# Kernel optimization log

Measured on AMD Instinct MI355X. Metric: run time of the kernel, lower is better.

## Reference

```python
import jax, jax.numpy as jnp
import numpy as np

LN_EPS = 1e-5


def _layernorm(x, g, b):
    m = x.mean(-1, keepdims=True)
    v = ((x - m) ** 2).mean(-1, keepdims=True)
    return (x - m) * jax.lax.rsqrt(v + LN_EPS) * g + b


def setup_inputs() -> dict:
    key = jax.random.key(0)
    ks = jax.random.split(key, 8)
    bs, dsc, qlen, dm, nh, dc, dff = 16, 8, 512, 256, 16, 128, 1024
    dk = dm // nh  # 16
    s = 0.02
    return {
        "src": jax.random.normal(ks[0], (bs, dsc, qlen, dm), jnp.float32),
        "router": jax.random.normal(ks[1], (1, nh, dc, dk), jnp.float32) * 0.1,
        "Wk_w": jax.random.normal(ks[2], (nh * dk, dm), jnp.float32) * s,
        "Wk_b": jnp.zeros((nh * dk,), jnp.float32),
        "out_w": jax.random.normal(ks[3], (dm, nh * dk), jnp.float32) * s,
        "out_b": jnp.zeros((dm,), jnp.float32),
        "m_expand": jax.random.normal(ks[4], (1, qlen, dc), jnp.float32) * 0.1,
        "pos_embd": jax.random.normal(ks[5], (1, 1, dc, dm), jnp.float32) * 0.02,
        "scale_tf": jnp.ones((1, dsc, 1, 1), jnp.float32),
        "ln1_g": jnp.ones((dm,), jnp.float32),
        "ln1_b": jnp.zeros((dm,), jnp.float32),
        "ff1_w": jax.random.normal(ks[6], (dff, dm), jnp.float32) * s,
        "ff1_b": jnp.zeros((dff,), jnp.float32),
        "ff2_w": jax.random.normal(ks[7], (dm, dff), jnp.float32) * s,
        "ff2_b": jnp.zeros((dm,), jnp.float32),
        "ln2_g": jnp.ones((dm,), jnp.float32),
        "ln2_b": jnp.zeros((dm,), jnp.float32),
    }


def reference(src, router, Wk_w, Wk_b, out_w, out_b, m_expand, pos_embd,
              scale_tf, ln1_g, ln1_b, ff1_w, ff1_b, ff2_w, ff2_b, ln2_g, ln2_b):
    bs, dsc, qlen, dm = src.shape
    _, nh, dc, dk = router.shape
    scale = jnp.asarray(dk, src.dtype) ** -0.5

    # flatten (d_share_corr, q_len) into attended sequence S = dsc*qlen
    x = src.reshape(bs, dsc * qlen, dm)
    k = (x @ Wk_w.T + Wk_b).reshape(bs, dsc * qlen, nh, dk)  # [b,S,h,dk]

    # learned-router compressed attention: Q = router (shared across batch), V = K (b_share_kv)
    scores = jnp.einsum('hcd,bshd->bhcs', router[0], k) * scale  # [b,h,dc,S]
    attn = jax.nn.softmax(scores, axis=-1)
    ctx = jnp.einsum('bhcs,bshd->bchd', attn, k).reshape(bs, dc, nh * dk)

    ar = (ctx @ out_w.T + out_b)[:, None] + pos_embd  # [b,1,dc,dm]

    # expand compressed tokens back to q_len, scale per transform
    src2 = jnp.einsum('qc,bxcd->bxqd', m_expand[0], ar) * scale_tf  # [b,dsc,q,dm]
    y = _layernorm(src + src2, ln1_g, ln1_b)

    # FFN (exact gelu, as torch default)
    h = jax.nn.gelu(y @ ff1_w.T + ff1_b, approximate=False)
    y = _layernorm(y + (h @ ff2_w.T + ff2_b), ln2_g, ln2_b)
    return y
```

## Files before the change

kernel.cpp:

```cpp
#include <hip/hip_runtime.h>
#include <math.h>

typedef unsigned short u16;
typedef unsigned int u32;
typedef __bf16 b16x8 __attribute__((ext_vector_type(8)));
typedef float f32x4 __attribute__((ext_vector_type(4)));

#define BS 16
#define DSC 8
#define QL 512
#define DM 256
#define NH 16
#define DKH 16
#define DC 128
#define DFF 1024
#define S_TOT 4096
#define R_TOT 65536
#define ATT_SCALE 0.36067376022224085f

static __device__ __forceinline__ u16 f2bf(float f) {
  u32 u = __float_as_uint(f);
  u += 0x7fffu + ((u >> 16) & 1u);
  return (u16)(u >> 16);
}

static __device__ __forceinline__ uint4 pack8(float4 a, float4 b) {
  uint4 o;
  o.x = (u32)f2bf(a.x) | ((u32)f2bf(a.y) << 16);
  o.y = (u32)f2bf(a.z) | ((u32)f2bf(a.w) << 16);
  o.z = (u32)f2bf(b.x) | ((u32)f2bf(b.y) << 16);
  o.w = (u32)f2bf(b.z) | ((u32)f2bf(b.w) << 16);
  return o;
}

__global__ void cvt_kernel(const float* __restrict__ in, u16* __restrict__ outp, int n4) {
  for (int i = blockIdx.x * blockDim.x + threadIdx.x; i < n4; i += gridDim.x * blockDim.x) {
    float4 v = *(const float4*)(in + (size_t)i * 4);
    uint2 o;
    o.x = (u32)f2bf(v.x) | ((u32)f2bf(v.y) << 16);
    o.y = (u32)f2bf(v.z) | ((u32)f2bf(v.w) << 16);
    *(uint2*)(outp + (size_t)i * 4) = o;
  }
}

__global__ void transp_kernel(const float* __restrict__ w, float* __restrict__ wt) {
  int i = blockIdx.x * 256 + threadIdx.x;
  int k = i >> 8, n = i & 255;
  wt[i] = w[n * 256 + k];
}

template <int EPI, int AF32, int NTY>
__global__ __launch_bounds__(256) void gemm_bf16(
    const void* __restrict__ Av, const u16* __restrict__ B,
    const float* __restrict__ bias, const float* __restrict__ resid,
    void* __restrict__ out, int K, int ldo) {
  __shared__ __align__(16) u16 As[128 * 40];
  __shared__ __align__(16) u16 Bs[128 * 40];
  const int g = blockIdx.x;
  const int xcd = g & 7, tt = g >> 3;
  const int m0 = (xcd * 64 + tt / NTY) * 128;
  const int n0 = (tt % NTY) * 128;
  const int tid = threadIdx.x;
  const int w = tid >> 6, lane = tid & 63;
  const int wm = (w >> 1) * 64, wn = (w & 1) * 64;
  const int fr = lane & 15, fq = lane >> 4;

  f32x4 acc[4][4];
#pragma unroll
  for (int i = 0; i < 4; i++)
#pragma unroll
    for (int j = 0; j < 4; j++) acc[i][j] = (f32x4){0.f, 0.f, 0.f, 0.f};

  const u16* Bg = B + (size_t)n0 * K;
  const int r0 = tid >> 2, o0 = (tid & 3) * 8;
  const int r1 = r0 + 64;

  for (int k0 = 0; k0 < K; k0 += 32) {
    uint4 a0, a1;
    if (AF32) {
      const float* Agf = (const float*)Av + (size_t)m0 * K;
      float4 l0 = *(const float4*)(Agf + (size_t)r0 * K + k0 + o0);
      float4 h0 = *(const float4*)(Agf + (size_t)r0 * K + k0 + o0 + 4);
      float4 l1 = *(const float4*)(Agf + (size_t)r1 * K + k0 + o0);
      float4 h1 = *(const float4*)(Agf + (size_t)r1 * K + k0 + o0 + 4);
      a0 = pack8(l0, h0);
      a1 = pack8(l1, h1);
    } else {
      const u16* Ag = (const u16*)Av + (size_t)m0 * K;
      a0 = *(const uint4*)(Ag + (size_t)r0 * K + k0 + o0);
      a1 = *(const uint4*)(Ag + (size_t)r1 * K + k0 + o0);
    }
    uint4 b0 = *(const uint4*)(Bg + (size_t)r0 * K + k0 + o0);
    uint4 b1 = *(const uint4*)(Bg + (size_t)r1 * K + k0 + o0);
    __syncthreads();
    *(uint4*)&As[r0 * 40 + o0] = a0;
    *(uint4*)&As[r1 * 40 + o0] = a1;
    *(uint4*)&Bs[r0 * 40 + o0] = b0;
    *(uint4*)&Bs[r1 * 40 + o0] = b1;
    __syncthreads();

    uint4 af[4], bf[4];
#pragma unroll
    for (int i = 0; i < 4; i++) {
      af[i] = *(const uint4*)&As[(wm + i * 16 + fr) * 40 + fq * 8];
      bf[i] = *(const uint4*)&Bs[(wn + i * 16 + fr) * 40 + fq * 8];
    }
#pragma unroll
    for (int mi = 0; mi < 4; mi++)
#pragma unroll
      for (int ni = 0; ni < 4; ni++)
        acc[mi][ni] = __builtin_amdgcn_mfma_f32_16x16x32_bf16(
            __builtin_bit_cast(b16x8, af[mi]), __builtin_bit_cast(b16x8, bf[ni]),
            acc[mi][ni], 0, 0, 0);
  }

#pragma unroll
  for (int ni = 0; ni < 4; ni++) {
    const int gc = n0 + wn + ni * 16 + fr;
    const float bv = bias[gc];
#pragma unroll
    for (int mi = 0; mi < 4; mi++) {
#pragma unroll
      for (int r = 0; r < 4; r++) {
        const int gr = m0 + wm + mi * 16 + fq * 4 + r;
        float v = acc[mi][ni][r] + bv;
        if (EPI == 1) v = 0.5f * v * (1.f + erff(v * 0.70710678118f));
        if (EPI == 2) {
          v += resid[(size_t)gr * ldo + gc];
          ((float*)out)[(size_t)gr * ldo + gc] = v;
        } else {
          ((u16*)out)[(size_t)gr * ldo + gc] = f2bf(v);
        }
      }
    }
  }
}

__global__ __launch_bounds__(256) void attn_mfma(const u16* __restrict__ kbf,
                                                 const float* __restrict__ router,
                                                 float* __restrict__ ctxb) {
  const int blk = blockIdx.x;
  const int bh = blk >> 1, chalf = blk & 1;
  const int b = bh >> 4, h = bh & 15;
  const int tid = threadIdx.x, w = tid >> 6, lane = tid & 63;
  const int l15 = lane & 15, lg = lane >> 4;

  __shared__ __align__(16) u16 Pl[4][64 * 40];
  __shared__ __align__(16) u16 kTl[4][16 * 40];
  __shared__ float ctxp[4][64][16];
  __shared__ float lp[4][64];

  uint4 rB[4];
  {
    const float* rb = router + ((size_t)h * DC + chalf * 64) * 16;
#pragma unroll
    for (int nf = 0; nf < 4; nf++) {
      if (lg < 2) {
        const float* p = rb + (nf * 16 + l15) * 16 + lg * 8;
        float4 lo = *(const float4*)p;
        float4 hi = *(const float4*)(p + 4);
        lo.x *= ATT_SCALE; lo.y *= ATT_SCALE; lo.z *= ATT_SCALE; lo.w *= ATT_SCALE;
        hi.x *= ATT_SCALE; hi.y *= ATT_SCALE; hi.z *= ATT_SCALE; hi.w *= ATT_SCALE;
        rB[nf] = pack8(lo, hi);
      } else {
        rB[nf] = make_uint4(0, 0, 0, 0);
      }
    }
  }

  const u16* kg = kbf + (size_t)b * S_TOT * (NH * DKH) + h * 16;

  f32x4 ctx[4];
#pragma unroll
  for (int i = 0; i < 4; i++) ctx[i] = (f32x4){0.f, 0.f, 0.f, 0.f};
  float ladd[4] = {0.f, 0.f, 0.f, 0.f};

  for (int tt = w; tt < 128; tt += 4) {
    const int s0 = tt * 32;
    uint4 kA[2];
#pragma unroll
    for (int mf = 0; mf < 2; mf++)
      kA[mf] = (lg < 2)
                   ? *(const uint4*)(kg + (size_t)(s0 + mf * 16 + l15) * 256 + lg * 8)
                   : make_uint4(0, 0, 0, 0);
    {
      const int sl = lane & 31, dh = lane >> 5;
      uint4 kv = *(const uint4*)(kg + (size_t)(s0 + sl) * 256 + dh * 8);
      const u16* pv = (const u16*)&kv;
#pragma unroll
      for (int jj = 0; jj < 8; jj++) kTl[w][(dh * 8 + jj) * 40 + sl] = pv[jj];
    }
    f32x4 sc[2][4];
#pragma unroll
    for (int mf = 0; mf < 2; mf++)
#pragma unroll
      for (int nf = 0; nf < 4; nf++)
        sc[mf][nf] = __builtin_amdgcn_mfma_f32_16x16x32_bf16(
            __builtin_bit_cast(b16x8, kA[mf]), __builtin_bit_cast(b16x8, rB[nf]),
            (f32x4){0.f, 0.f, 0.f, 0.f}, 0, 0, 0);
#pragma unroll
    for (int mf = 0; mf < 2; mf++)
#pragma unroll
      for (int nf = 0; nf < 4; nf++) {
        float p0 = exp2f(sc[mf][nf][0]);
        float p1 = exp2f(sc[mf][nf][1]);
        float p2 = exp2f(sc[mf][nf][2]);
        float p3 = exp2f(sc[mf][nf][3]);
        ladd[nf] += (p0 + p1) + (p2 + p3);
        uint2 pk;
        pk.x = (__float_as_uint(p0) >> 16) | (__float_as_uint(p1) & 0xffff0000u);
        pk.y = (__float_as_uint(p2) >> 16) | (__float_as_uint(p3) & 0xffff0000u);
        *(uint2*)&Pl[w][(nf * 16 + l15) * 40 + mf * 16 + lg * 4] = pk;
      }
    uint4 kB = *(const uint4*)&kTl[w][l15 * 40 + lg * 8];
#pragma unroll
    for (int mfc = 0; mfc < 4; mfc++) {
      uint4 pA = *(const uint4*)&Pl[w][(mfc * 16 + l15) * 40 + lg * 8];
      ctx[mfc] = __builtin_amdgcn_mfma_f32_16x16x32_bf16(
          __builtin_bit_cast(b16x8, pA), __builtin_bit_cast(b16x8, kB), ctx[mfc],
          0, 0, 0);
    }
  }

#pragma unroll
  for (int nf = 0; nf < 4; nf++) {
    float v = ladd[nf];
    v += __shfl_xor(v, 16);
    v += __shfl_xor(v, 32);
    ladd[nf] = v;
  }
  if (lane < 16) {
#pragma unroll
    for (int nf = 0; nf < 4; nf++) lp[w][nf * 16 + lane] = ladd[nf];
  }
#pragma unroll
  for (int mfc = 0; mfc < 4; mfc++)
#pragma unroll
    for (int r = 0; r < 4; r++) ctxp[w][mfc * 16 + lg * 4 + r][l15] = ctx[mfc][r];
  __syncthreads();
#pragma unroll
  for (int i = 0; i < 4; i++) {
    const int idx = tid + i * 256;
    const int c = idx >> 4, d = idx & 15;
    const float L = lp[0][c] + lp[1][c] + lp[2][c] + lp[3][c];
    const float V = ctxp[0][c][d] + ctxp[1][c][d] + ctxp[2][c][d] + ctxp[3][c][d];
    ctxb[((size_t)b * DC + chalf * 64 + c) * (NH * DKH) + h * 16 + d] = V / L;
  }
}

__global__ __launch_bounds__(256) void ar_kernel(const float* __restrict__ ctxb,
                                                 const float* __restrict__ owT,
                                                 const float* __restrict__ ob,
                                                 const float* __restrict__ pos,
                                                 float* __restrict__ ar) {
  const int b = blockIdx.x, g = blockIdx.y, n = threadIdx.x;
  __shared__ float cl[8][256];
#pragma unroll
  for (int j = 0; j < 8; j++)
    cl[j][n] = ctxb[((size_t)b * DC + g * 8 + j) * 256 + n];
  __syncthreads();
  float acc[8];
#pragma unroll
  for (int j = 0; j < 8; j++) acc[j] = ob[n] + pos[(size_t)(g * 8 + j) * 256 + n];
  for (int k = 0; k < 256; k++) {
    float wv = owT[(size_t)k * 256 + n];
#pragma unroll
    for (int j = 0; j < 8; j++) acc[j] += cl[j][k] * wv;
  }
#pragma unroll
  for (int j = 0; j < 8; j++) ar[((size_t)b * DC + g * 8 + j) * 256 + n] = acc[j];
}

__global__ __launch_bounds__(256) void texp_kernel(const float* __restrict__ me,
                                                   const float* __restrict__ ar,
                                                   float* __restrict__ tb) {
  const int b = blockIdx.x, qg = blockIdx.y, d = threadIdx.x;
  __shared__ float ml[16][128];
  const int q0 = qg * 16;
  for (int i = threadIdx.x; i < 16 * 128; i += 256) {
    int qq = i >> 7, c = i & 127;
    ml[qq][c] = me[(size_t)(q0 + qq) * 128 + c];
  }
  __syncthreads();
  float acc[16];
#pragma unroll
  for (int qq = 0; qq < 16; qq++) acc[qq] = 0.f;
  for (int c = 0; c < 128; c++) {
    float v = ar[((size_t)b * DC + c) * 256 + d];
#pragma unroll
    for (int qq = 0; qq < 16; qq++) acc[qq] += ml[qq][c] * v;
  }
#pragma unroll
  for (int qq = 0; qq < 16; qq++)
    tb[((size_t)(b * QL + q0 + qq)) * 256 + d] = acc[qq];
}

__global__ __launch_bounds__(256) void ln1_kernel(
    const float* __restrict__ src, const float* __restrict__ tbuf,
    const float* __restrict__ stf, const float* __restrict__ g,
    const float* __restrict__ bb, float* __restrict__ yout) {
  const int w = threadIdx.x >> 6, lane = threadIdx.x & 63;
  const int r = blockIdx.x * 4 + w;
  const int b = r >> 12, x = (r >> 9) & 7, q = r & 511;
  const size_t base = (size_t)r * DM + lane * 4;
  float4 s4 = *(const float4*)(src + base);
  float4 t4 = *(const float4*)(tbuf + ((size_t)(b * QL + q) * DM + lane * 4));
  const float sc = stf[x];
  float v0 = s4.x + sc * t4.x, v1 = s4.y + sc * t4.y;
  float v2 = s4.z + sc * t4.z, v3 = s4.w + sc * t4.w;
  float sum = v0 + v1 + v2 + v3;
  float sq = v0 * v0 + v1 * v1 + v2 * v2 + v3 * v3;
#pragma unroll
  for (int off = 32; off; off >>= 1) {
    sum += __shfl_xor(sum, off);
    sq += __shfl_xor(sq, off);
  }
  const float mean = sum * (1.f / DM);
  const float var = sq * (1.f / DM) - mean * mean;
  const float rs = rsqrtf(var + 1e-5f);
  float4 gv = *(const float4*)(g + lane * 4);
  float4 bv = *(const float4*)(bb + lane * 4);
  float4 o;
  o.x = (v0 - mean) * rs * gv.x + bv.x;
  o.y = (v1 - mean) * rs * gv.y + bv.y;
  o.z = (v2 - mean) * rs * gv.z + bv.z;
  o.w = (v3 - mean) * rs * gv.w + bv.w;
  *(float4*)(yout + base) = o;
}

__global__ __launch_bounds__(256) void ln2_kernel(float* __restrict__ io,
                                                  const float* __restrict__ g,
                                                  const float* __restrict__ bb) {
  const int w = threadIdx.x >> 6, lane = threadIdx.x & 63;
  const int r = blockIdx.x * 4 + w;
  const size_t base = (size_t)r * DM + lane * 4;
  float4 v4 = *(const float4*)(io + base);
  float sum = v4.x + v4.y + v4.z + v4.w;
  float sq = v4.x * v4.x + v4.y * v4.y + v4.z * v4.z + v4.w * v4.w;
#pragma unroll
  for (int off = 32; off; off >>= 1) {
    sum += __shfl_xor(sum, off);
    sq += __shfl_xor(sq, off);
  }
  const float mean = sum * (1.f / DM);
  const float var = sq * (1.f / DM) - mean * mean;
  const float rs = rsqrtf(var + 1e-5f);
  float4 gv = *(const float4*)(g + lane * 4);
  float4 bv = *(const float4*)(bb + lane * 4);
  float4 o;
  o.x = (v4.x - mean) * rs * gv.x + bv.x;
  o.y = (v4.y - mean) * rs * gv.y + bv.y;
  o.z = (v4.z - mean) * rs * gv.z + bv.z;
  o.w = (v4.w - mean) * rs * gv.w + bv.w;
  *(float4*)(io + base) = o;
}

extern "C" void kernel_launch(void* const* d_in, const int* in_sizes, int n_in,
                              void* d_out, int out_size, void* d_ws, size_t ws_size,
                              hipStream_t stream) {
  const float* src = (const float*)d_in[0];
  const float* router = (const float*)d_in[1];
  const float* wk_w = (const float*)d_in[2];
  const float* wk_b = (const float*)d_in[3];
  const float* out_w = (const float*)d_in[4];
  const float* out_b = (const float*)d_in[5];
  const float* m_exp = (const float*)d_in[6];
  const float* pos = (const float*)d_in[7];
  const float* stf = (const float*)d_in[8];
  const float* ln1g = (const float*)d_in[9];
  const float* ln1b = (const float*)d_in[10];
  const float* f1w = (const float*)d_in[11];
  const float* f1b = (const float*)d_in[12];
  const float* f2w = (const float*)d_in[13];
  const float* f2b = (const float*)d_in[14];
  const float* ln2g = (const float*)d_in[15];
  const float* ln2b = (const float*)d_in[16];
  float* out = (float*)d_out;

  unsigned char* ws = (unsigned char*)d_ws;
  u16* k_bf = (u16*)(ws + 0);
  u16* h_bf = (u16*)(ws + 33554432);
  u16* wkw_bf = (u16*)(ws + 167772160);
  u16* f1w_bf = (u16*)(ws + 167903232);
  u16* f2w_bf = (u16*)(ws + 168427520);
  float* owT = (float*)(ws + 168951808);
  float* ctxb = (float*)(ws + 169213952);
  float* arb = (float*)(ws + 171311104);
  float* tb = (float*)(ws + 173408256);

  cvt_kernel<<<64, 256, 0, stream>>>(wk_w, wkw_bf, 256 * 256 / 4);
  cvt_kernel<<<256, 256, 0, stream>>>(f1w, f1w_bf, DFF * DM / 4);
  cvt_kernel<<<256, 256, 0, stream>>>(f2w, f2w_bf, DM * DFF / 4);
  transp_kernel<<<256, 256, 0, stream>>>(out_w, owT);

  gemm_bf16<0, 1, 2><<<1024, 256, 0, stream>>>(src, wkw_bf, wk_b, nullptr,
                                               k_bf, DM, DM);
  attn_mfma<<<512, 256, 0, stream>>>(k_bf, router, ctxb);
  ar_kernel<<<dim3(16, 16), 256, 0, stream>>>(ctxb, owT, out_b, pos, arb);
  texp_kernel<<<dim3(16, 32), 256, 0, stream>>>(m_exp, arb, tb);
  ln1_kernel<<<16384, 256, 0, stream>>>(src, tb, stf, ln1g, ln1b, out);

  gemm_bf16<1, 1, 8><<<4096, 256, 0, stream>>>(out, f1w_bf, f1b, nullptr,
                                               h_bf, DM, DFF);
  gemm_bf16<2, 0, 2><<<1024, 256, 0, stream>>>(h_bf, f2w_bf, f2b, out,
                                               out, DFF, DM);
  ln2_kernel<<<16384, 256, 0, stream>>>(out, ln2g, ln2b);
}
```

Before: 492.3 us.

## Load GEMM tiles via global_load_lds, pre-convert A to bf16, stage output stores

The GEMM now loads A and B tiles straight into LDS with global_load_lds, which drops the register round trip and one barrier per k-step. To make that possible, the fp32 A operands are converted to bf16 up front: src gets a new conversion pass, and ln1 writes a bf16 copy of its output. The bf16 epilogue is staged through LDS so global stores are coalesced 16-byte writes. The cost is an extra full read and write of src, an extra bf16 write in ln1, and an unpadded LDS layout that may cause bank conflicts.

```diff
diff --git a/kernel.cpp b/kernel.cpp
--- a/kernel.cpp
+++ b/kernel.cpp
@@ -33,6 +33,12 @@
   return o;
 }
 
+static __device__ __forceinline__ void gload16(const u16* g, u16* l) {
+  __builtin_amdgcn_global_load_lds(
+      (const __attribute__((address_space(1))) void*)g,
+      (__attribute__((address_space(3))) void*)l, 16, 0, 0);
+}
+
 __global__ void cvt_kernel(const float* __restrict__ in, u16* __restrict__ outp, int n4) {
   for (int i = blockIdx.x * blockDim.x + threadIdx.x; i < n4; i += gridDim.x * blockDim.x) {
     float4 v = *(const float4*)(in + (size_t)i * 4);
@@ -49,13 +55,14 @@
   wt[i] = w[n * 256 + k];
 }
 
-template <int EPI, int AF32, int NTY>
+template <int EPI, int NTY>
 __global__ __launch_bounds__(256) void gemm_bf16(
-    const void* __restrict__ Av, const u16* __restrict__ B,
+    const u16* __restrict__ A, const u16* __restrict__ B,
     const float* __restrict__ bias, const float* __restrict__ resid,
     void* __restrict__ out, int K, int ldo) {
-  __shared__ __align__(16) u16 As[128 * 40];
-  __shared__ __align__(16) u16 Bs[128 * 40];
+  __shared__ __align__(16) u16 smem[8192];
+  u16* As = smem;
+  u16* Bs = smem + 4096;
   const int g = blockIdx.x;
   const int xcd = g & 7, tt = g >> 3;
   const int m0 = (xcd * 64 + tt / NTY) * 128;
@@ -71,39 +78,30 @@
 #pragma unroll
     for (int j = 0; j < 4; j++) acc[i][j] = (f32x4){0.f, 0.f, 0.f, 0.f};
 
+  const int jr = lane >> 2, jc = (lane & 3) * 8;
+  const u16* Ag = A + (size_t)m0 * K;
   const u16* Bg = B + (size_t)n0 * K;
-  const int r0 = tid >> 2, o0 = (tid & 3) * 8;
-  const int r1 = r0 + 64;
+  const u16* ga0 = Ag + (size_t)((2 * w) * 16 + jr) * K + jc;
+  const u16* ga1 = Ag + (size_t)((2 * w + 1) * 16 + jr) * K + jc;
+  const u16* gb0 = Bg + (size_t)((2 * w) * 16 + jr) * K + jc;
+  const u16* gb1 = Bg + (size_t)((2 * w + 1) * 16 + jr) * K + jc;
+  u16* la0 = As + (2 * w) * 512;
+  u16* la1 = As + (2 * w + 1) * 512;
+  u16* lb0 = Bs + (2 * w) * 512;
+  u16* lb1 = Bs + (2 * w + 1) * 512;
 
   for (int k0 = 0; k0 < K; k0 += 32) {
-    uint4 a0, a1;
-    if (AF32) {
-      const float* Agf = (const float*)Av + (size_t)m0 * K;
-      float4 l0 = *(const float4*)(Agf + (size_t)r0 * K + k0 + o0);
-      float4 h0 = *(const float4*)(Agf + (size_t)r0 * K + k0 + o0 + 4);
-      float4 l1 = *(const float4*)(Agf + (size_t)r1 * K + k0 + o0);
-      float4 h1 = *(const float4*)(Agf + (size_t)r1 * K + k0 + o0 + 4);
-      a0 = pack8(l0, h0);
-      a1 = pack8(l1, h1);
-    } else {
-      const u16* Ag = (const u16*)Av + (size_t)m0 * K;
-      a0 = *(const uint4*)(Ag + (size_t)r0 * K + k0 + o0);
-      a1 = *(const uint4*)(Ag + (size_t)r1 * K + k0 + o0);
-    }
-    uint4 b0 = *(const uint4*)(Bg + (size_t)r0 * K + k0 + o0);
-    uint4 b1 = *(const uint4*)(Bg + (size_t)r1 * K + k0 + o0);
+    gload16(ga0 + k0, la0);
+    gload16(ga1 + k0, la1);
+    gload16(gb0 + k0, lb0);
+    gload16(gb1 + k0, lb1);
     __syncthreads();
-    *(uint4*)&As[r0 * 40 + o0] = a0;
-    *(uint4*)&As[r1 * 40 + o0] = a1;
-    *(uint4*)&Bs[r0 * 40 + o0] = b0;
-    *(uint4*)&Bs[r1 * 40 + o0] = b1;
-    __syncthreads();
 
     uint4 af[4], bf[4];
 #pragma unroll
     for (int i = 0; i < 4; i++) {
-      af[i] = *(const uint4*)&As[(wm + i * 16 + fr) * 40 + fq * 8];
-      bf[i] = *(const uint4*)&Bs[(wn + i * 16 + fr) * 40 + fq * 8];
+      af[i] = *(const uint4*)&As[(wm + i * 16 + fr) * 32 + fq * 8];
+      bf[i] = *(const uint4*)&Bs[(wn + i * 16 + fr) * 32 + fq * 8];
     }
 #pragma unroll
     for (int mi = 0; mi < 4; mi++)
@@ -112,26 +110,51 @@
         acc[mi][ni] = __builtin_amdgcn_mfma_f32_16x16x32_bf16(
             __builtin_bit_cast(b16x8, af[mi]), __builtin_bit_cast(b16x8, bf[ni]),
             acc[mi][ni], 0, 0, 0);
-  }
-
-#pragma unroll
-  for (int ni = 0; ni < 4; ni++) {
-    const int gc = n0 + wn + ni * 16 + fr;
-    const float bv = bias[gc];
-#pragma unroll
-    for (int mi = 0; mi < 4; mi++) {
-#pragma unroll
-      for (int r = 0; r < 4; r++) {
-        const int gr = m0 + wm + mi * 16 + fq * 4 + r;
-        float v = acc[mi][ni][r] + bv;
-        if (EPI == 1) v = 0.5f * v * (1.f + erff(v * 0.70710678118f));
-        if (EPI == 2) {
-          v += resid[(size_t)gr * ldo + gc];
+    __syncthreads();
+  }
+
+  if (EPI == 2) {
+#pragma unroll
+    for (int ni = 0; ni < 4; ni++) {
+      const int gc = n0 + wn + ni * 16 + fr;
+      const float bv = bias[gc];
+#pragma unroll
+      for (int mi = 0; mi < 4; mi++) {
+#pragma unroll
+        for (int r = 0; r < 4; r++) {
+          const int gr = m0 + wm + mi * 16 + fq * 4 + r;
+          float v = acc[mi][ni][r] + bv + resid[(size_t)gr * ldo + gc];
           ((float*)out)[(size_t)gr * ldo + gc] = v;
-        } else {
-          ((u16*)out)[(size_t)gr * ldo + gc] = f2bf(v);
         }
       }
+    }
+  } else {
+#pragma unroll
+    for (int h = 0; h < 2; h++) {
+      if ((w >> 1) == h) {
+#pragma unroll
+        for (int ni = 0; ni < 4; ni++) {
+          const float bv = bias[n0 + wn + ni * 16 + fr];
+#pragma unroll
+          for (int mi = 0; mi < 4; mi++) {
+#pragma unroll
+            for (int r = 0; r < 4; r++) {
+              float v = acc[mi][ni][r] + bv;
+              if (EPI == 1) v = 0.5f * v * (1.f + erff(v * 0.70710678118f));
+              smem[(mi * 16 + fq * 4 + r) * 128 + wn + ni * 16 + fr] = f2bf(v);
+            }
+          }
+        }
+      }
+      __syncthreads();
+#pragma unroll
+      for (int cc = 0; cc < 4; cc++) {
+        const int idx = tid + cc * 256;
+        const int row = idx >> 4, c16 = idx & 15;
+        uint4 v = *(const uint4*)&smem[row * 128 + c16 * 8];
+        *(uint4*)((u16*)out + (size_t)(m0 + h * 64 + row) * ldo + n0 + c16 * 8) = v;
+      }
+      __syncthreads();
     }
   }
 }
@@ -298,7 +321,7 @@
 __global__ __launch_bounds__(256) void ln1_kernel(
     const float* __restrict__ src, const float* __restrict__ tbuf,
     const float* __restrict__ stf, const float* __restrict__ g,
-    const float* __restrict__ bb, float* __restrict__ yout) {
+    const float* __restrict__ bb, float* __restrict__ yout, u16* __restrict__ ybf) {
   const int w = threadIdx.x >> 6, lane = threadIdx.x & 63;
   const int r = blockIdx.x * 4 + w;
   const int b = r >> 12, x = (r >> 9) & 7, q = r & 511;
@@ -320,12 +343,16 @@
   const float rs = rsqrtf(var + 1e-5f);
   float4 gv = *(const float4*)(g + lane * 4);
   float4 bv = *(const float4*)(bb + lane * 4);
-  float4 o;
-  o.x = (v0 - mean) * rs * gv.x + bv.x;
-  o.y = (v1 - mean) * rs * gv.y + bv.y;
-  o.z = (v2 - mean) * rs * gv.z + bv.z;
-  o.w = (v3 - mean) * rs * gv.w + bv.w;
+  float o0 = (v0 - mean) * rs * gv.x + bv.x;
+  float o1 = (v1 - mean) * rs * gv.y + bv.y;
+  float o2 = (v2 - mean) * rs * gv.z + bv.z;
+  float o3 = (v3 - mean) * rs * gv.w + bv.w;
+  float4 o = {o0, o1, o2, o3};
   *(float4*)(yout + base) = o;
+  uint2 p;
+  p.x = (u32)f2bf(o0) | ((u32)f2bf(o1) << 16);
+  p.y = (u32)f2bf(o2) | ((u32)f2bf(o3) << 16);
+  *(uint2*)(ybf + base) = p;
 }
 
 __global__ __launch_bounds__(256) void ln2_kernel(float* __restrict__ io,
@@ -378,31 +405,34 @@
   float* out = (float*)d_out;
 
   unsigned char* ws = (unsigned char*)d_ws;
-  u16* k_bf = (u16*)(ws + 0);
-  u16* h_bf = (u16*)(ws + 33554432);
-  u16* wkw_bf = (u16*)(ws + 167772160);
-  u16* f1w_bf = (u16*)(ws + 167903232);
-  u16* f2w_bf = (u16*)(ws + 168427520);
-  float* owT = (float*)(ws + 168951808);
-  float* ctxb = (float*)(ws + 169213952);
-  float* arb = (float*)(ws + 171311104);
-  float* tb = (float*)(ws + 173408256);
-
+  u16* h_bf = (u16*)(ws + 0);
+  u16* src_bf = (u16*)(ws + 0);
+  u16* y_bf = (u16*)(ws + 134217728);
+  u16* k_bf = (u16*)(ws + 167772160);
+  u16* wkw_bf = (u16*)(ws + 201326592);
+  u16* f1w_bf = (u16*)(ws + 201457664);
+  u16* f2w_bf = (u16*)(ws + 201981952);
+  float* owT = (float*)(ws + 202506240);
+  float* ctxb = (float*)(ws + 202768384);
+  float* arb = (float*)(ws + 204865536);
+  float* tb = (float*)(ws + 206962688);
+
+  cvt_kernel<<<2048, 256, 0, stream>>>(src, src_bf, R_TOT * DM / 4);
   cvt_kernel<<<64, 256, 0, stream>>>(wk_w, wkw_bf, 256 * 256 / 4);
   cvt_kernel<<<256, 256, 0, stream>>>(f1w, f1w_bf, DFF * DM / 4);
   cvt_kernel<<<256, 256, 0, stream>>>(f2w, f2w_bf, DM * DFF / 4);
   transp_kernel<<<256, 256, 0, stream>>>(out_w, owT);
 
-  gemm_bf16<0, 1, 2><<<1024, 256, 0, stream>>>(src, wkw_bf, wk_b, nullptr,
-                                               k_bf, DM, DM);
+  gemm_bf16<0, 2><<<1024, 256, 0, stream>>>(src_bf, wkw_bf, wk_b, nullptr,
+                                            k_bf, DM, DM);
   attn_mfma<<<512, 256, 0, stream>>>(k_bf, router, ctxb);
   ar_kernel<<<dim3(16, 16), 256, 0, stream>>>(ctxb, owT, out_b, pos, arb);
   texp_kernel<<<dim3(16, 32), 256, 0, stream>>>(m_exp, arb, tb);
-  ln1_kernel<<<16384, 256, 0, stream>>>(src, tb, stf, ln1g, ln1b, out);
-
-  gemm_bf16<1, 1, 8><<<4096, 256, 0, stream>>>(out, f1w_bf, f1b, nullptr,
-                                               h_bf, DM, DFF);
-  gemm_bf16<2, 0, 2><<<1024, 256, 0, stream>>>(h_bf, f2w_bf, f2b, out,
-                                               out, DFF, DM);
+  ln1_kernel<<<16384, 256, 0, stream>>>(src, tb, stf, ln1g, ln1b, out, y_bf);
+
+  gemm_bf16<1, 8><<<4096, 256, 0, stream>>>(y_bf, f1w_bf, f1b, nullptr,
+                                            h_bf, DM, DFF);
+  gemm_bf16<2, 2><<<1024, 256, 0, stream>>>(h_bf, f2w_bf, f2b, out,
+                                            out, DFF, DM);
   ln2_kernel<<<16384, 256, 0, stream>>>(out, ln2g, ln2b);
 }
```

Measured after the change: 503.8 us. 2.3% more time.
